# Optimization experiments

Measured on AMD Instinct MI355X. Metric: run time of the kernel, lower is better.

Reference implementation:

```python
import jax, jax.numpy as jnp
import numpy as np
import math

NUM_HEADS = 8
RES_K = 9  # depthwise conv kernel size along token axis

@jax.custom_vjp
def sign_ste(x):
    # binary quantization with straight-through estimator (EcoformerQuant)
    return jnp.sign(x)

def _ste_fwd(x):
    return jnp.sign(x), None

def _ste_bwd(_, g):
    return (g,)

sign_ste.defvjp(_ste_fwd, _ste_bwd)


def setup_inputs() -> dict:
    key = jax.random.key(0)
    ks = jax.random.split(key, 7)
    B, N, C = 8, 4096, 384
    nh = NUM_HEADS
    D = C // nh          # head_dim = 48
    F = D                # nb_features defaults to head_dim
    w = lambda k, shape: (jax.random.normal(k, shape, jnp.float32) * 0.02)
    return {
        "x": jax.random.normal(ks[0], (B, N, C), jnp.float32),
        "w_qk": w(ks[1], (C, C)),          # nn.Linear(dim, dim, bias=False)
        "w_v": w(ks[2], (C, C)),           # nn.Linear(dim, dim, bias=False)
        "w_proj": w(ks[3], (C, C)),        # nn.Linear(dim, dim)
        "b_proj": jnp.zeros((C,), jnp.float32),
        "hash_proj": jax.random.normal(ks[4], (nh, F, D), jnp.float32),  # EcoformerQuant projection
        "w_dconv": w(ks[5], (nh, 1, RES_K, 1)),  # depthwise Conv2d weight [out, in/groups, kh, kw]
        "H": 64,
        "W": 64,
    }


def reference(x, w_qk, w_v, w_proj, b_proj, hash_proj, w_dconv, H, W):
    B, N, C = x.shape
    nh = NUM_HEADS
    D = C // nh
    # projections -> [B, heads, N, head_dim]
    qk = (x @ w_qk.T).reshape(B, N, nh, D).transpose(0, 2, 1, 3)
    v = (x @ w_v.T).reshape(B, N, nh, D).transpose(0, 2, 1, 3)
    # L2-normalize along head_dim (angular kernel)
    qk = qk / jnp.linalg.norm(qk, axis=-1, keepdims=True)
    # EcoformerQuant: per-head hash projection + binary codes, scaled to ~unit norm
    codes = sign_ste(jnp.einsum('bhnd,hfd->bhnf', qk, hash_proj))
    codes = codes / jnp.sqrt(jnp.asarray(codes.shape[-1], x.dtype))
    # depthwise conv over token axis, shared across head_dim (kernel (9,1), pad (4,0))
    dconv_v = jax.lax.conv_general_dilated(
        v, w_dconv, window_strides=(1, 1), padding=((RES_K // 2, RES_K // 2), (0, 0)),
        dimension_numbers=('NCHW', 'OIHW', 'NCHW'), feature_group_count=nh)
    # linear (associative) attention: (codes^T v) first -> [B, h, F, D]
    attn = jnp.einsum('bhnf,bhnd->bhfd', codes, v)
    out = 0.5 * v + (1.0 / math.pi) * jnp.einsum('bhnf,bhfd->bhnd', codes, attn)
    out = out / jnp.linalg.norm(out, axis=-1, keepdims=True)
    out = out + dconv_v
    out = out.transpose(0, 2, 1, 3).reshape(B, N, C)
    return out @ w_proj.T + b_proj
```

## Files before the change

### kernel.cpp

```cpp
#include <hip/hip_runtime.h>

#define B_   8
#define N_   4096
#define C_   384
#define NH_  8
#define HD_  48
#define M_   (B_ * N_)


__global__ __launch_bounds__(256) void prep_w1(const float* __restrict__ w_qk,
                                               const float* __restrict__ w_v,
                                               float* __restrict__ W1)
{
    int idx = blockIdx.x * 256 + threadIdx.x;
    int k = idx / 768, n = idx % 768;
    W1[idx] = (n < 384) ? w_qk[(size_t)n * 384 + k]
                        : w_v[(size_t)(n - 384) * 384 + k];
}

__global__ __launch_bounds__(256) void prep_w3(const float* __restrict__ w_proj,
                                               float* __restrict__ W3)
{
    int idx = blockIdx.x * 256 + threadIdx.x;
    int k = idx / 384, n = idx % 384;
    W3[idx] = w_proj[n * 384 + k];
}

__global__ __launch_bounds__(256) void zerok(float* __restrict__ p, int n)
{
    int i = blockIdx.x * 256 + threadIdx.x;
    if (i < n) p[i] = 0.f;
}


#define BM 128
#define BN 64
#define BK 32

template <int EPI>
__global__ __launch_bounds__(256) void gemm_f32(const float* __restrict__ A,
                                                const float* __restrict__ Bm,
                                                const float* __restrict__ bias,
                                                float* __restrict__ out0,
                                                float* __restrict__ out1,
                                                int N, int K)
{
    __shared__ float As[BK][BM + 4];
    __shared__ float Bs[BK][BN];
    const int t    = threadIdx.x;
    const int row0 = blockIdx.x * BM;
    const int col0 = blockIdx.y * BN;
    const int tm   = t >> 4;
    const int tn   = t & 15;

    float acc[8][4];
    #pragma unroll
    for (int i = 0; i < 8; ++i)
        #pragma unroll
        for (int j = 0; j < 4; ++j) acc[i][j] = 0.f;

    const float* Ab = A + (size_t)row0 * K;

    for (int k0 = 0; k0 < K; k0 += BK) {
        __syncthreads();
        #pragma unroll
        for (int it = 0; it < 4; ++it) {
            int idx = it * 256 + t;
            int ar = idx >> 3, aq = idx & 7;
            float4 va = *(const float4*)(Ab + (size_t)ar * K + k0 + aq * 4);
            As[aq * 4 + 0][ar] = va.x;
            As[aq * 4 + 1][ar] = va.y;
            As[aq * 4 + 2][ar] = va.z;
            As[aq * 4 + 3][ar] = va.w;
        }
        #pragma unroll
        for (int it = 0; it < 2; ++it) {
            int idx = it * 256 + t;
            int br = idx >> 4, bq = idx & 15;
            *(float4*)&Bs[br][bq * 4] =
                *(const float4*)(Bm + (size_t)(k0 + br) * N + col0 + bq * 4);
        }
        __syncthreads();
        #pragma unroll
        for (int k = 0; k < BK; ++k) {
            float a[8], b[4];
            #pragma unroll
            for (int i = 0; i < 8; ++i) a[i] = As[k][tm * 8 + i];
            #pragma unroll
            for (int j = 0; j < 4; ++j) b[j] = Bs[k][tn * 4 + j];
            #pragma unroll
            for (int i = 0; i < 8; ++i)
                #pragma unroll
                for (int j = 0; j < 4; ++j)
                    acc[i][j] = fmaf(a[i], b[j], acc[i][j]);
        }
    }

    if (EPI == 0) {
        const bool isc = (col0 < 384);
        float* dst = isc ? out0 : out1;
        const int cc = (isc ? col0 : col0 - 384) + tn * 4;
        #pragma unroll
        for (int i = 0; i < 8; ++i) {
            int m = row0 + tm * 8 + i;
            float4 r;
            r.x = acc[i][0]; r.y = acc[i][1];
            r.z = acc[i][2]; r.w = acc[i][3];
            *(float4*)&dst[(size_t)m * 384 + cc] = r;
        }
    } else {
        float4 bb = *(const float4*)&bias[col0 + tn * 4];
        #pragma unroll
        for (int i = 0; i < 8; ++i) {
            int m = row0 + tm * 8 + i;
            float4 r;
            r.x = acc[i][0] + bb.x; r.y = acc[i][1] + bb.y;
            r.z = acc[i][2] + bb.z; r.w = acc[i][3] + bb.w;
            *(float4*)&out0[(size_t)m * 384 + col0 + tn * 4] = r;
        }
    }
}

__global__ __launch_bounds__(64) void codes_emu(float* __restrict__ zc,
                                                const float* __restrict__ hashp)
{
#pragma clang fp contract(off)
    const int bid  = blockIdx.x;
    const int row  = bid >> 3;
    const int h    = bid & 7;
    const int lane = threadIdx.x;

    __shared__ float q[48];
    __shared__ float qh[48];
    __shared__ float nrm_s;

    float* base = zc + (size_t)row * 384 + h * 48;
    if (lane < 48) q[lane] = base[lane];
    __syncthreads();

    if (lane == 0) {
        float r[8];
        #pragma unroll
        for (int j = 0; j < 8; ++j) r[j] = q[j] * q[j];
        #pragma unroll
        for (int i = 8; i < 48; i += 8)
            #pragma unroll
            for (int j = 0; j < 8; ++j) r[j] = r[j] + q[i + j] * q[i + j];
        float s = ((r[0] + r[1]) + (r[2] + r[3])) + ((r[4] + r[5]) + (r[6] + r[7]));
        nrm_s = sqrtf(s);
    }
    __syncthreads();
    if (lane < 48) qh[lane] = q[lane] / nrm_s;
    __syncthreads();

    if (lane < 48) {
        const float* hp = hashp + (size_t)h * 2304 + (size_t)lane * 48;
        float z = 0.f;
        #pragma unroll
        for (int i = 0; i < 48; ++i)
            z = fmaf(qh[i], hp[i], z);
        base[lane] = z > 0.f ? 1.f : (z < 0.f ? -1.f : 0.f);
    }
}

__global__ __launch_bounds__(256) void attn_k(const float* __restrict__ codes,
                                              const float* __restrict__ v,
                                              float* __restrict__ attn)
{
    const int bh = blockIdx.x;
    const int b = bh >> 3, h = bh & 7;
    const int n0 = blockIdx.y * 512;
    __shared__ float cs[128][48];
    __shared__ float vs[128][48];
    const int t = threadIdx.x;
    const int fi = (t >> 4) * 3;
    const int di = (t & 15) * 3;
    float acc[3][3];
    #pragma unroll
    for (int i = 0; i < 3; ++i)
        #pragma unroll
        for (int j = 0; j < 3; ++j) acc[i][j] = 0.f;

    const size_t base = ((size_t)b * N_) * C_ + h * 48;
    for (int c0 = 0; c0 < 512; c0 += 128) {
        __syncthreads();
        #pragma unroll
        for (int l = 0; l < 6; ++l) {
            int idx = l * 256 + t;
            int r = idx / 12, q = idx % 12;
            size_t g = base + (size_t)(n0 + c0 + r) * C_ + q * 4;
            *(float4*)&cs[r][q * 4] = *(const float4*)(codes + g);
            *(float4*)&vs[r][q * 4] = *(const float4*)(v + g);
        }
        __syncthreads();
        for (int nn = 0; nn < 128; ++nn) {
            float c0r = cs[nn][fi + 0], c1r = cs[nn][fi + 1], c2r = cs[nn][fi + 2];
            float v0 = vs[nn][di + 0], v1 = vs[nn][di + 1], v2 = vs[nn][di + 2];
            acc[0][0] = fmaf(c0r, v0, acc[0][0]);
            acc[0][1] = fmaf(c0r, v1, acc[0][1]);
            acc[0][2] = fmaf(c0r, v2, acc[0][2]);
            acc[1][0] = fmaf(c1r, v0, acc[1][0]);
            acc[1][1] = fmaf(c1r, v1, acc[1][1]);
            acc[1][2] = fmaf(c1r, v2, acc[1][2]);
            acc[2][0] = fmaf(c2r, v0, acc[2][0]);
            acc[2][1] = fmaf(c2r, v1, acc[2][1]);
            acc[2][2] = fmaf(c2r, v2, acc[2][2]);
        }
    }
    float* dst = attn + (size_t)bh * 2304;
    #pragma unroll
    for (int i = 0; i < 3; ++i)
        #pragma unroll
        for (int j = 0; j < 3; ++j)
            atomicAdd(&dst[(fi + i) * 48 + (di + j)], acc[i][j]);
}

__device__ __forceinline__ void fma_row(float c, const float* __restrict__ ar,
                                        float4* __restrict__ s4)
{
    #pragma unroll
    for (int q = 0; q < 12; ++q) {
        float4 a = *(const float4*)(ar + q * 4);
        s4[q].x = fmaf(c, a.x, s4[q].x);
        s4[q].y = fmaf(c, a.y, s4[q].y);
        s4[q].z = fmaf(c, a.z, s4[q].z);
        s4[q].w = fmaf(c, a.w, s4[q].w);
    }
}

__global__ __launch_bounds__(256) void out_k(const float* __restrict__ codes,
                                             const float* __restrict__ v,
                                             const float* __restrict__ attn,
                                             const float* __restrict__ wd,
                                             float* __restrict__ y)
{
    const int bh = blockIdx.x;
    const int b = bh >> 3, h = bh & 7;
    const int t = threadIdx.x;
    const int n = blockIdx.y * 256 + t;
    __shared__ float As[48][48];
    {
        const float* ap = attn + (size_t)bh * 2304;
        const float SC = 1.0f / (48.0f * 3.14159265358979323846f);
        #pragma unroll
        for (int l = 0; l < 9; ++l) {
            int idx = l * 256 + t;
            As[idx / 48][idx % 48] = ap[idx] * SC;
        }
    }
    float wdl[9];
    #pragma unroll
    for (int k = 0; k < 9; ++k) wdl[k] = wd[h * 9 + k];
    __syncthreads();

    const size_t rowbase = ((size_t)(b * N_ + n)) * C_ + h * 48;

    float4 s4[12];
    #pragma unroll
    for (int q = 0; q < 12; ++q) s4[q] = make_float4(0.f, 0.f, 0.f, 0.f);
    for (int fq = 0; fq < 12; ++fq) {
        float4 cf = *(const float4*)(codes + rowbase + fq * 4);
        const float* a0 = &As[fq * 4][0];
        fma_row(cf.x, a0,        s4);
        fma_row(cf.y, a0 + 48,   s4);
        fma_row(cf.z, a0 + 96,   s4);
        fma_row(cf.w, a0 + 144,  s4);
    }

    float4 o4[12];
    float nrm = 0.f;
    {
        const float* vr = v + rowbase;
        #pragma unroll
        for (int q = 0; q < 12; ++q) {
            float4 vv = *(const float4*)(vr + q * 4);
            o4[q].x = fmaf(0.5f, vv.x, s4[q].x);
            o4[q].y = fmaf(0.5f, vv.y, s4[q].y);
            o4[q].z = fmaf(0.5f, vv.z, s4[q].z);
            o4[q].w = fmaf(0.5f, vv.w, s4[q].w);
            nrm = fmaf(o4[q].x, o4[q].x, nrm);
            nrm = fmaf(o4[q].y, o4[q].y, nrm);
            nrm = fmaf(o4[q].z, o4[q].z, nrm);
            nrm = fmaf(o4[q].w, o4[q].w, nrm);
        }
    }
    const float rn = 1.0f / sqrtf(nrm);

    float4 dc4[12];
    #pragma unroll
    for (int q = 0; q < 12; ++q) dc4[q] = make_float4(0.f, 0.f, 0.f, 0.f);
    for (int k = 0; k < 9; ++k) {
        int nn = n + k - 4;
        if ((unsigned)nn < (unsigned)N_) {
            const float* vr = v + ((size_t)(b * N_ + nn)) * C_ + h * 48;
            float wk = wdl[k];
            #pragma unroll
            for (int q = 0; q < 12; ++q) {
                float4 vv = *(const float4*)(vr + q * 4);
                dc4[q].x = fmaf(wk, vv.x, dc4[q].x);
                dc4[q].y = fmaf(wk, vv.y, dc4[q].y);
                dc4[q].z = fmaf(wk, vv.z, dc4[q].z);
                dc4[q].w = fmaf(wk, vv.w, dc4[q].w);
            }
        }
    }

    float* yr = y + rowbase;
    #pragma unroll
    for (int q = 0; q < 12; ++q) {
        float4 r;
        r.x = fmaf(o4[q].x, rn, dc4[q].x);
        r.y = fmaf(o4[q].y, rn, dc4[q].y);
        r.z = fmaf(o4[q].z, rn, dc4[q].z);
        r.w = fmaf(o4[q].w, rn, dc4[q].w);
        *(float4*)&yr[q * 4] = r;
    }
}

extern "C" void kernel_launch(void* const* d_in, const int* in_sizes, int n_in,
                              void* d_out, int out_size, void* d_ws, size_t ws_size,
                              hipStream_t stream)
{
    const float* x      = (const float*)d_in[0];
    const float* w_qk   = (const float*)d_in[1];
    const float* w_v    = (const float*)d_in[2];
    const float* w_proj = (const float*)d_in[3];
    const float* b_proj = (const float*)d_in[4];
    const float* hashp  = (const float*)d_in[5];
    const float* wd     = (const float*)d_in[6];
    float* out = (float*)d_out;

    float* ws    = (float*)d_ws;
    float* W1    = ws;
    float* W3    = W1 + 294912;
    float* zc    = W3 + 147456;
    float* vbuf  = zc + 12582912;
    float* attn  = vbuf + 12582912;
    float* y     = attn + 147456;

    hipLaunchKernelGGL(prep_w1, dim3(1152), dim3(256), 0, stream, w_qk, w_v, W1);
    hipLaunchKernelGGL(prep_w3, dim3(576), dim3(256), 0, stream, w_proj, W3);
    hipLaunchKernelGGL(zerok, dim3(576), dim3(256), 0, stream, attn, 147456);

    hipLaunchKernelGGL((gemm_f32<0>), dim3(M_ / BM, 768 / BN), dim3(256), 0, stream,
                       x, W1, (const float*)nullptr, zc, vbuf, 768, 384);

    hipLaunchKernelGGL(codes_emu, dim3(262144), dim3(64), 0, stream, zc, hashp);

    hipLaunchKernelGGL(attn_k, dim3(64, 8), dim3(256), 0, stream, zc, vbuf, attn);
    hipLaunchKernelGGL(out_k, dim3(64, 16), dim3(256), 0, stream, zc, vbuf, attn, wd, y);

    hipLaunchKernelGGL((gemm_f32<1>), dim3(M_ / BM, 384 / BN), dim3(256), 0, stream,
                       y, W3, b_proj, out, (float*)nullptr, 384, 384);
}
```

Baseline: 779.3 us.

## Enlarge GEMM tile to 128x128 and batch hash-code kernel over 16 rows

The FP32 GEMM tile widens from 128x64 to 128x128 with an 8x8 per-thread accumulator, reading B from shared memory as float4 pairs and storing A row-major with padding. The hash-code kernel now handles 16 rows per 256-thread block, staging the per-head hash projection in shared memory once per block instead of having each 64-thread block read it from global memory for a single row. This removes tiny-block launch overhead and repeated global loads of the projection, at the cost of more registers per GEMM thread, which may lower occupancy.

```diff
diff --git a/kernel.cpp b/kernel.cpp
--- a/kernel.cpp
+++ b/kernel.cpp
@@ -8,6 +8,7 @@
 #define M_   (B_ * N_)
 
 
+
 __global__ __launch_bounds__(256) void prep_w1(const float* __restrict__ w_qk,
                                                const float* __restrict__ w_v,
                                                float* __restrict__ W1)
@@ -34,18 +35,18 @@
 
 
 #define BM 128
-#define BN 64
+#define BN 128
 #define BK 32
 
 template <int EPI>
-__global__ __launch_bounds__(256) void gemm_f32(const float* __restrict__ A,
-                                                const float* __restrict__ Bm,
-                                                const float* __restrict__ bias,
-                                                float* __restrict__ out0,
-                                                float* __restrict__ out1,
-                                                int N, int K)
-{
-    __shared__ float As[BK][BM + 4];
+__global__ __launch_bounds__(256, 4) void gemm_f32(const float* __restrict__ A,
+                                                   const float* __restrict__ Bm,
+                                                   const float* __restrict__ bias,
+                                                   float* __restrict__ out0,
+                                                   float* __restrict__ out1,
+                                                   int N, int K)
+{
+    __shared__ float As[BM][BK + 1];
     __shared__ float Bs[BK][BN];
     const int t    = threadIdx.x;
     const int row0 = blockIdx.x * BM;
@@ -53,11 +54,11 @@
     const int tm   = t >> 4;
     const int tn   = t & 15;
 
-    float acc[8][4];
+    float acc[8][8];
     #pragma unroll
     for (int i = 0; i < 8; ++i)
         #pragma unroll
-        for (int j = 0; j < 4; ++j) acc[i][j] = 0.f;
+        for (int j = 0; j < 8; ++j) acc[i][j] = 0.f;
 
     const float* Ab = A + (size_t)row0 * K;
 
@@ -68,30 +69,32 @@
             int idx = it * 256 + t;
             int ar = idx >> 3, aq = idx & 7;
             float4 va = *(const float4*)(Ab + (size_t)ar * K + k0 + aq * 4);
-            As[aq * 4 + 0][ar] = va.x;
-            As[aq * 4 + 1][ar] = va.y;
-            As[aq * 4 + 2][ar] = va.z;
-            As[aq * 4 + 3][ar] = va.w;
-        }
-        #pragma unroll
-        for (int it = 0; it < 2; ++it) {
+            As[ar][aq * 4 + 0] = va.x;
+            As[ar][aq * 4 + 1] = va.y;
+            As[ar][aq * 4 + 2] = va.z;
+            As[ar][aq * 4 + 3] = va.w;
+        }
+        #pragma unroll
+        for (int it = 0; it < 4; ++it) {
             int idx = it * 256 + t;
-            int br = idx >> 4, bq = idx & 15;
+            int br = idx >> 5, bq = idx & 31;
             *(float4*)&Bs[br][bq * 4] =
                 *(const float4*)(Bm + (size_t)(k0 + br) * N + col0 + bq * 4);
         }
         __syncthreads();
         #pragma unroll
         for (int k = 0; k < BK; ++k) {
-            float a[8], b[4];
+            float a[8], b[8];
             #pragma unroll
-            for (int i = 0; i < 8; ++i) a[i] = As[k][tm * 8 + i];
-            #pragma unroll
-            for (int j = 0; j < 4; ++j) b[j] = Bs[k][tn * 4 + j];
+            for (int i = 0; i < 8; ++i) a[i] = As[tm * 8 + i][k];
+            float4 b0 = *(const float4*)&Bs[k][tn * 4];
+            float4 b1 = *(const float4*)&Bs[k][tn * 4 + 64];
+            b[0] = b0.x; b[1] = b0.y; b[2] = b0.z; b[3] = b0.w;
+            b[4] = b1.x; b[5] = b1.y; b[6] = b1.z; b[7] = b1.w;
             #pragma unroll
             for (int i = 0; i < 8; ++i)
                 #pragma unroll
-                for (int j = 0; j < 4; ++j)
+                for (int j = 0; j < 8; ++j)
                     acc[i][j] = fmaf(a[i], b[j], acc[i][j]);
         }
     }
@@ -103,63 +106,79 @@
         #pragma unroll
         for (int i = 0; i < 8; ++i) {
             int m = row0 + tm * 8 + i;
-            float4 r;
-            r.x = acc[i][0]; r.y = acc[i][1];
-            r.z = acc[i][2]; r.w = acc[i][3];
-            *(float4*)&dst[(size_t)m * 384 + cc] = r;
+            float4 r0, r1;
+            r0.x = acc[i][0]; r0.y = acc[i][1]; r0.z = acc[i][2]; r0.w = acc[i][3];
+            r1.x = acc[i][4]; r1.y = acc[i][5]; r1.z = acc[i][6]; r1.w = acc[i][7];
+            *(float4*)&dst[(size_t)m * 384 + cc]      = r0;
+            *(float4*)&dst[(size_t)m * 384 + cc + 64] = r1;
         }
     } else {
-        float4 bb = *(const float4*)&bias[col0 + tn * 4];
+        float4 bb0 = *(const float4*)&bias[col0 + tn * 4];
+        float4 bb1 = *(const float4*)&bias[col0 + tn * 4 + 64];
         #pragma unroll
         for (int i = 0; i < 8; ++i) {
             int m = row0 + tm * 8 + i;
-            float4 r;
-            r.x = acc[i][0] + bb.x; r.y = acc[i][1] + bb.y;
-            r.z = acc[i][2] + bb.z; r.w = acc[i][3] + bb.w;
-            *(float4*)&out0[(size_t)m * 384 + col0 + tn * 4] = r;
-        }
-    }
-}
-
-__global__ __launch_bounds__(64) void codes_emu(float* __restrict__ zc,
-                                                const float* __restrict__ hashp)
+            float4 r0, r1;
+            r0.x = acc[i][0] + bb0.x; r0.y = acc[i][1] + bb0.y;
+            r0.z = acc[i][2] + bb0.z; r0.w = acc[i][3] + bb0.w;
+            r1.x = acc[i][4] + bb1.x; r1.y = acc[i][5] + bb1.y;
+            r1.z = acc[i][6] + bb1.z; r1.w = acc[i][7] + bb1.w;
+            *(float4*)&out0[(size_t)m * 384 + col0 + tn * 4]      = r0;
+            *(float4*)&out0[(size_t)m * 384 + col0 + tn * 4 + 64] = r1;
+        }
+    }
+}
+
+__global__ __launch_bounds__(256) void codes_emu(float* __restrict__ zc,
+                                                 const float* __restrict__ hashp)
 {
 #pragma clang fp contract(off)
-    const int bid  = blockIdx.x;
-    const int row  = bid >> 3;
-    const int h    = bid & 7;
-    const int lane = threadIdx.x;
-
-    __shared__ float q[48];
-    __shared__ float qh[48];
-    __shared__ float nrm_s;
-
-    float* base = zc + (size_t)row * 384 + h * 48;
-    if (lane < 48) q[lane] = base[lane];
+    const int h  = blockIdx.y;
+    const int r0 = blockIdx.x * 16;
+    const int t  = threadIdx.x;
+
+    __shared__ float hs[48][49];
+    __shared__ float qh[16][49];
+    __shared__ float nrm_s[16];
+
+    for (int idx = t; idx < 2304; idx += 256)
+        hs[idx / 48][idx % 48] = hashp[(size_t)h * 2304 + idx];
+    for (int idx = t; idx < 768; idx += 256) {
+        int r = idx / 48, d = idx % 48;
+        qh[r][d] = zc[(size_t)(r0 + r) * 384 + h * 48 + d];
+    }
     __syncthreads();
 
-    if (lane == 0) {
+    if (t < 16) {
         float r[8];
         #pragma unroll
-        for (int j = 0; j < 8; ++j) r[j] = q[j] * q[j];
+        for (int j = 0; j < 8; ++j) r[j] = qh[t][j] * qh[t][j];
         #pragma unroll
         for (int i = 8; i < 48; i += 8)
             #pragma unroll
-            for (int j = 0; j < 8; ++j) r[j] = r[j] + q[i + j] * q[i + j];
+            for (int j = 0; j < 8; ++j) r[j] = r[j] + qh[t][i + j] * qh[t][i + j];
         float s = ((r[0] + r[1]) + (r[2] + r[3])) + ((r[4] + r[5]) + (r[6] + r[7]));
-        nrm_s = sqrtf(s);
+        nrm_s[t] = sqrtf(s);
     }
     __syncthreads();
-    if (lane < 48) qh[lane] = q[lane] / nrm_s;
+
+    for (int idx = t; idx < 768; idx += 256) {
+        int r = idx / 48, d = idx % 48;
+        qh[r][d] = qh[r][d] / nrm_s[r];
+    }
     __syncthreads();
 
-    if (lane < 48) {
-        const float* hp = hashp + (size_t)h * 2304 + (size_t)lane * 48;
+    const int r  = t >> 4;
+    const int fg = t & 15;
+    float* base = zc + (size_t)(r0 + r) * 384 + h * 48;
+    #pragma unroll
+    for (int j = 0; j < 3; ++j) {
+        int f = fg * 3 + j;
         float z = 0.f;
         #pragma unroll
         for (int i = 0; i < 48; ++i)
-            z = fmaf(qh[i], hp[i], z);
-        base[lane] = z > 0.f ? 1.f : (z < 0.f ? -1.f : 0.f);
+            z = fmaf(qh[r][i], hs[f][i], z);
+        base[f] = z > 0.f ? 1.f : (z < 0.f ? -1.f : 0.f);
     }
 }
 
@@ -345,7 +364,7 @@
     hipLaunchKernelGGL((gemm_f32<0>), dim3(M_ / BM, 768 / BN), dim3(256), 0, stream,
                        x, W1, (const float*)nullptr, zc, vbuf, 768, 384);
 
-    hipLaunchKernelGGL(codes_emu, dim3(262144), dim3(64), 0, stream, zc, hashp);
+    hipLaunchKernelGGL(codes_emu, dim3(M_ / 16, 8), dim3(256), 0, stream, zc, hashp);
 
     hipLaunchKernelGGL(attn_k, dim3(64, 8), dim3(256), 0, stream, zc, vbuf, attn);
     hipLaunchKernelGGL(out_k, dim3(64, 16), dim3(256), 0, stream, zc, vbuf, attn, wd, y);
```

Result: faster. 712.0 us (-8.6%).
